# Kernel optimization log

Hardware: AMD Instinct MI355X
Metric: run time of the kernel (lower is better)

Reference implementation:

```python
import jax, jax.numpy as jnp
import numpy as np

D_MODEL = 64
HEADS = 8
LEVELS = 5
POINTS = 4
DH = D_MODEL // HEADS
EPS = 1e-5


def _layernorm(x, g, b):
    m = x.mean(-1, keepdims=True)
    v = ((x - m) ** 2).mean(-1, keepdims=True)
    return (x - m) / jnp.sqrt(v + EPS) * g + b


def _bilinear_sample(v, lx, ly, Hl, Wl):
    # v: (B, heads, Hl, Wl, dh); lx, ly: (B, Nq, heads, P) normalized in ~[0,1]
    # matches F.grid_sample(align_corners=False, padding_mode='zeros')
    x = lx * Wl - 0.5
    y = ly * Hl - 0.5
    x0 = jnp.floor(x)
    y0 = jnp.floor(y)
    wx = x - x0
    wy = y - y0
    x0i = x0.astype(jnp.int32)
    y0i = y0.astype(jnp.int32)
    B, heads = v.shape[0], v.shape[1]
    bidx = jnp.arange(B)[:, None, None, None]
    hidx = jnp.arange(heads)[None, None, :, None]

    def gather(yi, xi):
        valid = (xi >= 0) & (xi < Wl) & (yi >= 0) & (yi < Hl)
        xc = jnp.clip(xi, 0, Wl - 1)
        yc = jnp.clip(yi, 0, Hl - 1)
        g = v[bidx, hidx, yc, xc]  # (B, Nq, heads, P, dh)
        return g * valid[..., None].astype(v.dtype)

    return (gather(y0i, x0i) * ((1 - wx) * (1 - wy))[..., None]
            + gather(y0i, x0i + 1) * (wx * (1 - wy))[..., None]
            + gather(y0i + 1, x0i) * ((1 - wx) * wy)[..., None]
            + gather(y0i + 1, x0i + 1) * (wx * wy)[..., None])


def setup_inputs() -> dict:
    key = jax.random.key(0)
    ks = jax.random.split(key, 24)
    B, NQ = 2, 20000
    ss = np.array([[184, 184], [92, 92], [46, 46], [23, 23], [12, 12]], dtype=np.int64)
    areas = ss[:, 0] * ss[:, 1]
    lsi = np.concatenate([[0], np.cumsum(areas)[:-1]]).astype(np.int64)
    LIN = int(areas.sum())  # 45109
    s = 0.02
    inp = {
        'q_feat': jax.random.normal(ks[0], (B, NQ, D_MODEL), jnp.float32),
        'dense_voxel_flatten': jax.random.normal(ks[1], (B, LIN, D_MODEL), jnp.float32),
        'reference_points': jax.random.uniform(ks[2], (B, NQ, 2), jnp.float32),
        'q_pos': jax.random.normal(ks[3], (B, NQ, D_MODEL), jnp.float32),
        'spatial_shapes': ss,
        'level_start_index': lsi,
        'Wv': jax.random.normal(ks[4], (D_MODEL, D_MODEL), jnp.float32) * s,
        'bv': jnp.zeros((D_MODEL,), jnp.float32),
        'Wo': jax.random.normal(ks[5], (D_MODEL, HEADS * LEVELS * POINTS * 2), jnp.float32) * s,
        'bo': jax.random.normal(ks[6], (HEADS * LEVELS * POINTS * 2,), jnp.float32),
        'Wa': jax.random.normal(ks[7], (D_MODEL, HEADS * LEVELS * POINTS), jnp.float32) * s,
        'ba': jnp.zeros((HEADS * LEVELS * POINTS,), jnp.float32),
        'Wout': jax.random.normal(ks[8], (D_MODEL, D_MODEL), jnp.float32) * s,
        'bout': jnp.zeros((D_MODEL,), jnp.float32),
        'g1': jnp.ones((D_MODEL,), jnp.float32),
        'b1': jnp.zeros((D_MODEL,), jnp.float32),
        'W1': jax.random.normal(ks[9], (D_MODEL, 1024), jnp.float32) * s,
        'bff1': jnp.zeros((1024,), jnp.float32),
        'W2': jax.random.normal(ks[10], (1024, D_MODEL), jnp.float32) * s,
        'bff2': jnp.zeros((D_MODEL,), jnp.float32),
        'g2': jnp.ones((D_MODEL,), jnp.float32),
        'b2': jnp.zeros((D_MODEL,), jnp.float32),
    }
    return inp


def reference(q_feat, dense_voxel_flatten, reference_points, q_pos,
              spatial_shapes, level_start_index,
              Wv, bv, Wo, bo, Wa, ba, Wout, bout,
              g1, b1, W1, bff1, W2, bff2, g2, b2):
    B, NQ, _ = q_feat.shape
    q = q_feat + q_pos  # with_pos_embed
    value = (dense_voxel_flatten @ Wv + bv).reshape(B, -1, HEADS, DH)
    off = (q @ Wo + bo).reshape(B, NQ, HEADS, LEVELS, POINTS, 2)
    aw = jax.nn.softmax((q @ Wa + ba).reshape(B, NQ, HEADS, LEVELS * POINTS), axis=-1)
    aw = aw.reshape(B, NQ, HEADS, LEVELS, POINTS)
    # offset normalizer is (W, H) per level
    ssn = np.asarray(spatial_shapes)
    normalizer = jnp.asarray(ssn[:, ::-1].copy(), q.dtype)  # (L, 2)
    loc = reference_points[:, :, None, None, None, :] + off / normalizer[None, None, None, :, None, :]
    out = jnp.zeros((B, NQ, HEADS, DH), q.dtype)
    for l in range(LEVELS):
        Hl, Wl = int(ssn[l, 0]), int(ssn[l, 1])
        st = int(np.asarray(level_start_index)[l])
        vl = value[:, st:st + Hl * Wl].reshape(B, Hl, Wl, HEADS, DH).transpose(0, 3, 1, 2, 4)
        sampled = _bilinear_sample(vl, loc[:, :, :, l, :, 0], loc[:, :, :, l, :, 1], Hl, Wl)
        out = out + jnp.einsum('bnhpd,bnhp->bnhd', sampled, aw[:, :, :, l])
    attn_out = out.reshape(B, NQ, D_MODEL) @ Wout + bout
    x = _layernorm(q_feat + attn_out, g1, b1)  # residual + norm1 (dropout=0)
    ffn = jax.nn.relu(x @ W1 + bff1) @ W2 + bff2
    return _layernorm(x + ffn, g2, b2)
```

## Files before the change

kernel.cpp:

```cpp
#include <hip/hip_runtime.h>
#include <hip/hip_bf16.h>

#define NB 2
#define NQ 20000
#define DM 64
#define NH 8
#define NL 5
#define NP 4
#define LIN 45109
#define FFN 1024

typedef __attribute__((ext_vector_type(8))) short short8;
typedef __attribute__((ext_vector_type(4))) float f32x4;

__device__ __forceinline__ float b2f(const __hip_bfloat16 h) { return __bfloat162float(h); }
__device__ __forceinline__ float lo16f(unsigned u) { return __uint_as_float(u << 16); }
__device__ __forceinline__ float hi16f(unsigned u) { return __uint_as_float(u & 0xffff0000u); }
__device__ __forceinline__ unsigned f2bf_bits(float x) {
    unsigned u = __float_as_uint(x);
    return (u + 0x7FFFu + ((u >> 16) & 1u)) >> 16;
}

__global__ void __launch_bounds__(256)
val_proj_kernel(const float* __restrict__ dvf,
                const float* __restrict__ Wv,
                const float* __restrict__ bv,
                __hip_bfloat16* __restrict__ valA,
                __hip_bfloat16* __restrict__ valB,
                int rows) {
    __shared__ __align__(16) __hip_bfloat16 wvp[8][64][8];
    __shared__ __align__(16) __hip_bfloat16 ar[64][72];
    __shared__ __align__(16) float bvs[64];

    const int tid = threadIdx.x;
    const int lane = tid & 63;
    const int w = tid >> 6;
    const int m16 = lane & 15, qd = lane >> 4;
    const int row0 = blockIdx.x * 64;

    for (int idx = tid; idx < 4096; idx += 256) {
        const int j = idx & 7;
        const int l = (idx >> 3) & 63;
        const int seg = idx >> 9;
        const int nt = seg >> 1, kc = seg & 1;
        const int n = nt * 16 + (l & 15);
        const int k = kc * 32 + (l >> 4) * 8 + j;
        wvp[seg][l][j] = __float2bfloat16(Wv[k * 64 + n]);
    }
    if (tid < 64) bvs[tid] = bv[tid];

    {
        const int r = w * 16 + m16;
        const int grow = row0 + r;
        const int c0 = qd * 16;
        __hip_bfloat16* dst = &ar[r][c0];
        if (grow < rows) {
            const float4* src = (const float4*)&dvf[(size_t)grow * DM + c0];
#pragma unroll
            for (int t = 0; t < 4; t++) {
                const float4 v = src[t];
                dst[t * 4 + 0] = __float2bfloat16(v.x);
                dst[t * 4 + 1] = __float2bfloat16(v.y);
                dst[t * 4 + 2] = __float2bfloat16(v.z);
                dst[t * 4 + 3] = __float2bfloat16(v.w);
            }
        } else {
#pragma unroll
            for (int t = 0; t < 16; t++) dst[t] = __float2bfloat16(0.f);
        }
    }
    __syncthreads();

    f32x4 acc[4];
#pragma unroll
    for (int nt = 0; nt < 4; nt++) acc[nt] = (f32x4){0.f, 0.f, 0.f, 0.f};
#pragma unroll
    for (int kc = 0; kc < 2; kc++) {
        const short8 a = *(const short8*)&ar[w * 16 + m16][kc * 32 + qd * 8];
#pragma unroll
        for (int nt = 0; nt < 4; nt++) {
            const short8 b = *(const short8*)&wvp[nt * 2 + kc][lane][0];
            acc[nt] = __builtin_amdgcn_mfma_f32_16x16x32_bf16(a, b, acc[nt], 0, 0, 0);
        }
    }

#pragma unroll
    for (int r = 0; r < 4; r++) {
        const int gr = row0 + w * 16 + qd * 4 + r;
        if (gr < rows) {
            const int vr = (gr < LIN) ? gr : gr - LIN;
            __hip_bfloat16* dst = (gr < LIN) ? valA : valB;
#pragma unroll
            for (int nt = 0; nt < 4; nt++) {
                const int c = nt * 16 + m16;
                dst[((size_t)(c >> 3) * LIN + vr) * 8 + (c & 7)] =
                    __float2bfloat16(acc[nt][r] + bvs[c]);
            }
        }
    }
}

__global__ void pack_kernel(const float* __restrict__ W1, const float* __restrict__ W2,
                            const float* __restrict__ Wo, const float* __restrict__ Wa,
                            const float* __restrict__ Wout,
                            __hip_bfloat16* __restrict__ W1p, __hip_bfloat16* __restrict__ W2p,
                            __hip_bfloat16* __restrict__ Woap, __hip_bfloat16* __restrict__ Woutp) {
    const int t = blockIdx.x * 256 + threadIdx.x;
    const int lane = t & 63;
    const int m = lane & 15, qd = lane >> 4;
    const int seg = t >> 6;
    if (seg < 128) {
        const int nt = seg >> 1, kc = seg & 1;
        const int n = nt * 16 + m, kb = kc * 32 + qd * 8;
        __hip_bfloat16* dst = W1p + ((size_t)seg * 64 + lane) * 8;
#pragma unroll
        for (int j = 0; j < 8; j++) dst[j] = __float2bfloat16(W1[(size_t)(kb + j) * FFN + n]);
    } else if (seg < 256) {
        const int sl = seg - 128;
        const int nt = sl >> 5, kc = sl & 31;
        const int n = nt * 16 + m, kb = kc * 32 + qd * 8;
        __hip_bfloat16* dst = W2p + ((size_t)sl * 64 + lane) * 8;
#pragma unroll
        for (int j = 0; j < 8; j++) dst[j] = __float2bfloat16(W2[(size_t)(kb + j) * DM + n]);
    } else if (seg < 316) {
        const int sl = seg - 256;
        const int nt = sl >> 1, kc = sl & 1;
        const int n = nt * 16 + m, kb = kc * 32 + qd * 8;
        __hip_bfloat16* dst = Woap + ((size_t)sl * 64 + lane) * 8;
#pragma unroll
        for (int j = 0; j < 8; j++) {
            const int k = kb + j;
            const float v = (n < 320) ? Wo[(size_t)k * 320 + n] : Wa[(size_t)k * 160 + (n - 320)];
            dst[j] = __float2bfloat16(v);
        }
    } else if (seg < 324) {
        const int sl = seg - 316;
        const int nt = sl >> 1, kc = sl & 1;
        const int n = nt * 16 + m, kb = kc * 32 + qd * 8;
        __hip_bfloat16* dst = Woutp + ((size_t)sl * 64 + lane) * 8;
#pragma unroll
        for (int j = 0; j < 8; j++) dst[j] = __float2bfloat16(Wout[(size_t)(kb + j) * DM + n]);
    }
}

__global__ void __launch_bounds__(256, 8)
attn4_kernel(const float* __restrict__ q_feat,
             const float* __restrict__ ref_pts,
             const float* __restrict__ q_pos,
             const __hip_bfloat16* __restrict__ Woap,
             const float* __restrict__ bo, const float* __restrict__ ba,
             const __hip_bfloat16* __restrict__ Woutp, const float* __restrict__ bout,
             const float* __restrict__ g1, const float* __restrict__ b1,
             const __hip_bfloat16* __restrict__ valA,
             const __hip_bfloat16* __restrict__ valB,
             int qoff,
             float* __restrict__ xout) {
    __shared__ __align__(16) __hip_bfloat16 qb[16][72];
    __shared__ __align__(16) float offs[4][321];
    __shared__ __align__(16) float aws[4][161];
    __shared__ __align__(16) float refs[4][2];
    __shared__ __align__(16) int   dbase[640];
    __shared__ __align__(16) uint2 dwp[640];
    __shared__ __align__(16) float xs4[4][64];

    const int tid = threadIdx.x;
    const int lane = tid & 63;
    const int w = tid >> 6;
    const int m16 = lane & 15, qd = lane >> 4;
    const int q0 = qoff + blockIdx.x * 4;
    const int qi = q0 + w;

    const int sz[NL]  = {184, 92, 46, 23, 12};
    const int lsi[NL] = {0, 33856, 42320, 44436, 44965};

    const __hip_bfloat16* valp = (q0 >= NQ) ? valB : valA;

    const float qf = q_feat[(size_t)qi * DM + lane];
    const float qp = q_pos[(size_t)qi * DM + lane];
    qb[w][lane] = __float2bfloat16(qf + qp);
    for (int idx = tid; idx < 12 * 64; idx += 256)
        qb[4 + (idx >> 6)][idx & 63] = __float2bfloat16(0.f);
    if (tid < 8) refs[tid >> 1][tid & 1] = ref_pts[(size_t)(q0 + (tid >> 1)) * 2 + (tid & 1)];
    __syncthreads();

    for (int nt = w; nt < 30; nt += 4) {
        f32x4 acc = {0.f, 0.f, 0.f, 0.f};
#pragma unroll
        for (int kc = 0; kc < 2; kc++) {
            const short8 a = *(const short8*)&qb[m16][kc * 32 + qd * 8];
            const short8 b = *(const short8*)(Woap + ((size_t)(nt * 2 + kc) * 64 + lane) * 8);
            acc = __builtin_amdgcn_mfma_f32_16x16x32_bf16(a, b, acc, 0, 0, 0);
        }
        if (qd == 0) {
            const int n = nt * 16 + m16;
            if (n < 320) {
                const float bn = bo[n];
#pragma unroll
                for (int r = 0; r < 4; r++) offs[r][n] = acc[r] + bn;
            } else {
                const float bn = ba[n - 320];
#pragma unroll
                for (int r = 0; r < 4; r++) aws[r][n - 320] = acc[r] + bn;
            }
        }
    }
    __syncthreads();

    {
        const int g = tid >> 3;
        const int q = g >> 3, h = g & 7;
        const int j = tid & 7;
        float* p = &aws[q][h * 20];
        const float v0 = p[j], v1 = p[j + 8];
        const float v2 = (j < 4) ? p[j + 16] : -1e30f;
        float mx = fmaxf(fmaxf(v0, v1), v2);
        mx = fmaxf(mx, __shfl_xor(mx, 1, 8));
        mx = fmaxf(mx, __shfl_xor(mx, 2, 8));
        mx = fmaxf(mx, __shfl_xor(mx, 4, 8));
        const float e0 = __expf(v0 - mx), e1 = __expf(v1 - mx);
        const float e2 = (j < 4) ? __expf(v2 - mx) : 0.f;
        float s = e0 + e1 + e2;
        s += __shfl_xor(s, 1, 8);
        s += __shfl_xor(s, 2, 8);
        s += __shfl_xor(s, 4, 8);
        const float inv = 1.f / s;
        p[j] = e0 * inv;
        p[j + 8] = e1 * inv;
        if (j < 4) p[j + 16] = e2 * inv;
    }
    __syncthreads();

    for (int s = tid; s < 640; s += 256) {
        const int h = s & 7;
        const int t2 = s >> 3;
        const int p = t2 & 3;
        const int t3 = t2 >> 2;
        const int l = t3 % 5;
        const int q = t3 / 5;
        const int Wl = sz[l];
        const float Wf = (float)Wl;
        const int st = lsi[l];
        const int c = ((h * 5 + l) * 4 + p) * 2;
        const float fx = fmaf(refs[q][0], Wf, offs[q][c]) - 0.5f;
        const float fy = fmaf(refs[q][1], Wf, offs[q][c + 1]) - 0.5f;
        const float x0f = floorf(fx), y0f = floorf(fy);
        const float wx = fx - x0f, wy = fy - y0f;
        const int x0 = (int)x0f, y0 = (int)y0f;
        const float aV = aws[q][h * 20 + l * 4 + p];
        const bool xin0 = (x0 >= 0) & (x0 < Wl);
        const bool xin1 = (x0 >= -1) & (x0 < Wl - 1);
        const bool yin0 = (y0 >= 0) & (y0 < Wl);
        const bool yin1 = (y0 >= -1) & (y0 < Wl - 1);
        const float w00 = (xin0 & yin0) ? (1.f - wx) * (1.f - wy) * aV : 0.f;
        const float w10 = (xin1 & yin0) ? wx * (1.f - wy) * aV : 0.f;
        const float w01 = (xin0 & yin1) ? (1.f - wx) * wy * aV : 0.f;
        const float w11 = (xin1 & yin1) ? wx * wy * aV : 0.f;
        int base = (st + y0 * Wl + x0) * 8;
        base = base < -1520 ? -1520 : base;
        base = base > LIN * 8 ? LIN * 8 : base;
        dbase[s] = base;
        uint2 dw;
        dw.x = f2bf_bits(w00) | (f2bf_bits(w10) << 16);
        dw.y = f2bf_bits(w01) | (f2bf_bits(w11) << 16);
        dwp[s] = dw;
    }
    __syncthreads();

    {
        const int h = lane >> 3, d = lane & 7;
        const __hip_bfloat16* vbase = valp + (size_t)h * (LIN * 8) + d;
        float a0 = 0.f, a1 = 0.f, a2 = 0.f, a3 = 0.f;
        const int wl8[NL] = {184 * 8, 92 * 8, 46 * 8, 23 * 8, 12 * 8};
#pragma unroll
        for (int l = 0; l < NL; l++) {
#pragma unroll
            for (int p = 0; p < NP; p++) {
                const int idx = ((w * 5 + l) * 4 + p) * 8 + h;
                const int base = dbase[idx];
                const uint2 dw = dwp[idx];
                const __hip_bfloat16* r0 = vbase + base;
                const __hip_bfloat16* r1 = r0 + wl8[l];
                a0 = fmaf(lo16f(dw.x), b2f(r0[0]), a0);
                a1 = fmaf(hi16f(dw.x), b2f(r0[8]), a1);
                a2 = fmaf(lo16f(dw.y), b2f(r1[0]), a2);
                a3 = fmaf(hi16f(dw.y), b2f(r1[8]), a3);
            }
        }
        qb[w][lane] = __float2bfloat16((a0 + a1) + (a2 + a3));
    }
    __syncthreads();

    {
        f32x4 acc = {0.f, 0.f, 0.f, 0.f};
#pragma unroll
        for (int kc = 0; kc < 2; kc++) {
            const short8 a = *(const short8*)&qb[m16][kc * 32 + qd * 8];
            const short8 b = *(const short8*)(Woutp + ((size_t)(w * 2 + kc) * 64 + lane) * 8);
            acc = __builtin_amdgcn_mfma_f32_16x16x32_bf16(a, b, acc, 0, 0, 0);
        }
        if (qd == 0) {
            const int n = w * 16 + m16;
            const float bn = bout[n];
#pragma unroll
            for (int r = 0; r < 4; r++) xs4[r][n] = acc[r] + bn;
        }
    }
    __syncthreads();

    {
        const float xpre = qf + xs4[w][lane];
        float s = xpre, s2 = xpre * xpre;
#pragma unroll
        for (int o = 32; o >= 1; o >>= 1) {
            s += __shfl_xor(s, o, 64);
            s2 += __shfl_xor(s2, o, 64);
        }
        const float mean = s * (1.f / 64.f);
        const float var = s2 * (1.f / 64.f) - mean * mean;
        const float xn = (xpre - mean) * rsqrtf(var + 1e-5f);
        xout[(size_t)qi * DM + lane] = xn * g1[lane] + b1[lane];
    }
}

__global__ void __launch_bounds__(256)
ffn_kernel(const __hip_bfloat16* __restrict__ W1p, const float* __restrict__ bff1,
           const __hip_bfloat16* __restrict__ W2p, const float* __restrict__ bff2,
           const float* __restrict__ g2, const float* __restrict__ b2,
           float* __restrict__ io) {
    __shared__ __align__(16) __hip_bfloat16 xb[32][72];
    __shared__ __align__(16) __hip_bfloat16 hb[32][264];
    __shared__ __align__(16) float yr[32][64];

    const int tid = threadIdx.x;
    const int lane = tid & 63;
    const int w = tid >> 6;
    const int m16 = lane & 15, qd = lane >> 4;
    const int q0 = blockIdx.x * 32;

    {
        const int q = tid >> 3, i = tid & 7;
        const float4 v0 = *(const float4*)&io[(size_t)(q0 + q) * DM + i * 8];
        const float4 v1 = *(const float4*)&io[(size_t)(q0 + q) * DM + i * 8 + 4];
        __hip_bfloat16* xp = &xb[q][i * 8];
        xp[0] = __float2bfloat16(v0.x); xp[1] = __float2bfloat16(v0.y);
        xp[2] = __float2bfloat16(v0.z); xp[3] = __float2bfloat16(v0.w);
        xp[4] = __float2bfloat16(v1.x); xp[5] = __float2bfloat16(v1.y);
        xp[6] = __float2bfloat16(v1.z); xp[7] = __float2bfloat16(v1.w);
    }
    __syncthreads();

    f32x4 yacc[2];
    yacc[0] = (f32x4){0.f, 0.f, 0.f, 0.f};
    yacc[1] = (f32x4){0.f, 0.f, 0.f, 0.f};

#pragma unroll
    for (int qtr = 0; qtr < 4; qtr++) {
#pragma unroll
        for (int ti = 0; ti < 4; ti++) {
            const int nt = qtr * 16 + w + ti * 4;
            f32x4 acc[2];
            acc[0] = (f32x4){0.f, 0.f, 0.f, 0.f};
            acc[1] = (f32x4){0.f, 0.f, 0.f, 0.f};
#pragma unroll
            for (int kc = 0; kc < 2; kc++) {
                const short8 b = *(const short8*)(W1p + ((size_t)(nt * 2 + kc) * 64 + lane) * 8);
#pragma unroll
                for (int mt = 0; mt < 2; mt++) {
                    const short8 a = *(const short8*)&xb[mt * 16 + m16][kc * 32 + qd * 8];
                    acc[mt] = __builtin_amdgcn_mfma_f32_16x16x32_bf16(a, b, acc[mt], 0, 0, 0);
                }
            }
            const int ncol = (nt - qtr * 16) * 16 + m16;
            const float bn = bff1[nt * 16 + m16];
#pragma unroll
            for (int mt = 0; mt < 2; mt++)
#pragma unroll
                for (int r = 0; r < 4; r++)
                    hb[mt * 16 + qd * 4 + r][ncol] = __float2bfloat16(fmaxf(acc[mt][r] + bn, 0.f));
        }
        __syncthreads();
#pragma unroll
        for (int kc2 = 0; kc2 < 8; kc2++) {
            const short8 b = *(const short8*)(W2p + ((size_t)(w * 32 + qtr * 8 + kc2) * 64 + lane) * 8);
#pragma unroll
            for (int mt = 0; mt < 2; mt++) {
                const short8 a = *(const short8*)&hb[mt * 16 + m16][kc2 * 32 + qd * 8];
                yacc[mt] = __builtin_amdgcn_mfma_f32_16x16x32_bf16(a, b, yacc[mt], 0, 0, 0);
            }
        }
        __syncthreads();
    }

    {
        const int n = w * 16 + m16;
        const float bn = bff2[n];
#pragma unroll
        for (int mt = 0; mt < 2; mt++)
#pragma unroll
            for (int r = 0; r < 4; r++) {
                const int mm = mt * 16 + qd * 4 + r;
                yr[mm][n] = yacc[mt][r] + bn;
            }
    }
    __syncthreads();

    {
        const int q = tid >> 3, i = tid & 7;
        const float4 x0 = *(const float4*)&io[(size_t)(q0 + q) * DM + i * 8];
        const float4 x1 = *(const float4*)&io[(size_t)(q0 + q) * DM + i * 8 + 4];
        float4 v0 = *(const float4*)&yr[q][i * 8];
        float4 v1 = *(const float4*)&yr[q][i * 8 + 4];
        v0.x += x0.x; v0.y += x0.y; v0.z += x0.z; v0.w += x0.w;
        v1.x += x1.x; v1.y += x1.y; v1.z += x1.z; v1.w += x1.w;
        float s = v0.x + v0.y + v0.z + v0.w + v1.x + v1.y + v1.z + v1.w;
        float s2 = v0.x * v0.x + v0.y * v0.y + v0.z * v0.z + v0.w * v0.w
                 + v1.x * v1.x + v1.y * v1.y + v1.z * v1.z + v1.w * v1.w;
#pragma unroll
        for (int o = 4; o >= 1; o >>= 1) { s += __shfl_xor(s, o, 64); s2 += __shfl_xor(s2, o, 64); }
        const float mean = s * (1.f / 64.f);
        const float var = s2 * (1.f / 64.f) - mean * mean;
        const float rstd = rsqrtf(var + 1e-5f);
        const float4 ga = *(const float4*)&g2[i * 8];
        const float4 gb = *(const float4*)&g2[i * 8 + 4];
        const float4 ba4 = *(const float4*)&b2[i * 8];
        const float4 bb4 = *(const float4*)&b2[i * 8 + 4];
        float4 o0, o1;
        o0.x = (v0.x - mean) * rstd * ga.x + ba4.x;
        o0.y = (v0.y - mean) * rstd * ga.y + ba4.y;
        o0.z = (v0.z - mean) * rstd * ga.z + ba4.z;
        o0.w = (v0.w - mean) * rstd * ga.w + ba4.w;
        o1.x = (v1.x - mean) * rstd * gb.x + bb4.x;
        o1.y = (v1.y - mean) * rstd * gb.y + bb4.y;
        o1.z = (v1.z - mean) * rstd * gb.z + bb4.z;
        o1.w = (v1.w - mean) * rstd * gb.w + bb4.w;
        *(float4*)&io[(size_t)(q0 + q) * DM + i * 8] = o0;
        *(float4*)&io[(size_t)(q0 + q) * DM + i * 8 + 4] = o1;
    }
}

extern "C" void kernel_launch(void* const* d_in, const int* in_sizes, int n_in,
                              void* d_out, int out_size, void* d_ws, size_t ws_size,
                              hipStream_t stream) {
    const int B0 = (in_sizes[4] >= 4096) ? 4 : 6;
    const float* q_feat = (const float*)d_in[0];
    const float* dvf    = (const float*)d_in[1];
    const float* refp   = (const float*)d_in[2];
    const float* q_pos  = (const float*)d_in[3];
    const float* Wv   = (const float*)d_in[B0 + 0];
    const float* bv   = (const float*)d_in[B0 + 1];
    const float* Wo   = (const float*)d_in[B0 + 2];
    const float* bo   = (const float*)d_in[B0 + 3];
    const float* Wa   = (const float*)d_in[B0 + 4];
    const float* ba   = (const float*)d_in[B0 + 5];
    const float* Wout = (const float*)d_in[B0 + 6];
    const float* bout = (const float*)d_in[B0 + 7];
    const float* g1   = (const float*)d_in[B0 + 8];
    const float* b1   = (const float*)d_in[B0 + 9];
    const float* W1   = (const float*)d_in[B0 + 10];
    const float* bff1 = (const float*)d_in[B0 + 11];
    const float* W2   = (const float*)d_in[B0 + 12];
    const float* bff2 = (const float*)d_in[B0 + 13];
    const float* g2   = (const float*)d_in[B0 + 14];
    const float* b2   = (const float*)d_in[B0 + 15];
    float* out = (float*)d_out;

    const size_t val_elems = (size_t)LIN * DM;
    const size_t pack_elems = (size_t)(128 + 128 + 60 + 8) * 64 * 8;
    const size_t PAD_ELEMS = 12288;
    const bool dbuf = ws_size >= (pack_elems + 2 * val_elems + PAD_ELEMS) * sizeof(__hip_bfloat16);

    __hip_bfloat16* W1p = (__hip_bfloat16*)d_ws;
    __hip_bfloat16* W2p = W1p + (size_t)128 * 64 * 8;
    __hip_bfloat16* Woap = W2p + (size_t)128 * 64 * 8;
    __hip_bfloat16* Woutp = Woap + (size_t)60 * 64 * 8;
    __hip_bfloat16* val0 = W1p + pack_elems;
    __hip_bfloat16* val1 = dbuf ? val0 + val_elems : val0;

    __hip_bfloat16* pad_ptr = val1 + val_elems;
    hipMemsetAsync(pad_ptr, 0, PAD_ELEMS * sizeof(__hip_bfloat16), stream);

    pack_kernel<<<81, 256, 0, stream>>>(W1, W2, Wo, Wa, Wout, W1p, W2p, Woap, Woutp);

    if (dbuf) {
        val_proj_kernel<<<(2 * LIN + 63) / 64, 256, 0, stream>>>(
            dvf, Wv, bv, val0, val1, 2 * LIN);
        attn4_kernel<<<(NB * NQ) / 4, 256, 0, stream>>>(
            q_feat, refp, q_pos, Woap, bo, ba, Woutp, bout, g1, b1,
            val0, val1, 0, out);
    } else {
        for (int b = 0; b < NB; b++) {
            val_proj_kernel<<<(LIN + 63) / 64, 256, 0, stream>>>(
                dvf + (size_t)b * val_elems, Wv, bv, val0, val0, LIN);
            attn4_kernel<<<NQ / 4, 256, 0, stream>>>(
                q_feat, refp, q_pos, Woap, bo, ba, Woutp, bout, g1, b1,
                val0, val0, b * NQ, out);
        }
    }
    ffn_kernel<<<(NB * NQ) / 32, 256, 0, stream>>>(W1p, bff1, W2p, bff2, g2, b2, out);
}
```

Baseline: 251.3 us.

## Vectorize bilinear corner gathers to 16-byte loads with shuffle reduction

Before, each lane loaded one bf16 per corner, 80 scalar gathers in total. Now each lane loads a full 8-channel bf16 vector for one corner of one sample point, so each query-head needs 10 wide loads. Partial sums are combined with xor shuffles across 8 lanes and a select. The per-sample descriptor is packed into a single int4 and xs4 is aliased onto offs to cut LDS use. In exchange, 8-wide accumulators add register pressure and 24 shuffles per lane are added.

```diff
diff --git a/kernel.cpp b/kernel.cpp
--- a/kernel.cpp
+++ b/kernel.cpp
@@ -159,9 +159,9 @@
     __shared__ __align__(16) float offs[4][321];
     __shared__ __align__(16) float aws[4][161];
     __shared__ __align__(16) float refs[4][2];
-    __shared__ __align__(16) int   dbase[640];
-    __shared__ __align__(16) uint2 dwp[640];
-    __shared__ __align__(16) float xs4[4][64];
+    __shared__ __align__(16) int4  dsc[640];
+
+    float (*xs4)[64] = (float(*)[64])offs;
 
     const int tid = threadIdx.x;
     const int lane = tid & 63;
@@ -255,38 +255,46 @@
         const float w10 = (xin1 & yin0) ? wx * (1.f - wy) * aV : 0.f;
         const float w01 = (xin0 & yin1) ? (1.f - wx) * wy * aV : 0.f;
         const float w11 = (xin1 & yin1) ? wx * wy * aV : 0.f;
-        int base = (st + y0 * Wl + x0) * 8;
-        base = base < -1520 ? -1520 : base;
-        base = base > LIN * 8 ? LIN * 8 : base;
-        dbase[s] = base;
-        uint2 dw;
-        dw.x = f2bf_bits(w00) | (f2bf_bits(w10) << 16);
-        dw.y = f2bf_bits(w01) | (f2bf_bits(w11) << 16);
-        dwp[s] = dw;
-    }
-    __syncthreads();
-
-    {
-        const int h = lane >> 3, d = lane & 7;
-        const __hip_bfloat16* vbase = valp + (size_t)h * (LIN * 8) + d;
-        float a0 = 0.f, a1 = 0.f, a2 = 0.f, a3 = 0.f;
-        const int wl8[NL] = {184 * 8, 92 * 8, 46 * 8, 23 * 8, 12 * 8};
-#pragma unroll
-        for (int l = 0; l < NL; l++) {
-#pragma unroll
-            for (int p = 0; p < NP; p++) {
-                const int idx = ((w * 5 + l) * 4 + p) * 8 + h;
-                const int base = dbase[idx];
-                const uint2 dw = dwp[idx];
-                const __hip_bfloat16* r0 = vbase + base;
-                const __hip_bfloat16* r1 = r0 + wl8[l];
-                a0 = fmaf(lo16f(dw.x), b2f(r0[0]), a0);
-                a1 = fmaf(hi16f(dw.x), b2f(r0[8]), a1);
-                a2 = fmaf(lo16f(dw.y), b2f(r1[0]), a2);
-                a3 = fmaf(hi16f(dw.y), b2f(r1[8]), a3);
-            }
-        }
-        qb[w][lane] = __float2bfloat16((a0 + a1) + (a2 + a3));
+        int b0 = (st + y0 * Wl + x0) * 8;
+        b0 = b0 < -1520 ? -1520 : b0;
+        b0 = b0 > LIN * 8 ? LIN * 8 : b0;
+        const int b1 = b0 + Wl * 8;
+        int4 d4;
+        d4.x = b0;
+        d4.y = b1;
+        d4.z = (int)(f2bf_bits(w00) | (f2bf_bits(w10) << 16));
+        d4.w = (int)(f2bf_bits(w01) | (f2bf_bits(w11) << 16));
+        dsc[s] = d4;
+    }
+    __syncthreads();
+
+    {
+        const int h = lane >> 3, j = lane & 7;
+        const int c = j & 3;
+        const int sp = j >> 2;
+        const __hip_bfloat16* vbase = valp + (size_t)h * (LIN * 8);
+        float acc[8] = {0.f, 0.f, 0.f, 0.f, 0.f, 0.f, 0.f, 0.f};
+#pragma unroll
+        for (int k = 0; k < 10; k++) {
+            const int s = 2 * k + sp;
+            const int4 d4 = dsc[(w * 20 + s) * 8 + h];
+            const int base = (c >= 2) ? d4.y : d4.x;
+            const unsigned wb = (unsigned)((c >= 2) ? d4.w : d4.z);
+            const float wt = (c & 1) ? hi16f(wb) : lo16f(wb);
+            const short8 v = *(const short8*)(vbase + base + (c & 1) * 8);
+#pragma unroll
+            for (int d = 0; d < 8; d++)
+                acc[d] = fmaf(wt, __uint_as_float(((unsigned)(unsigned short)v[d]) << 16), acc[d]);
+        }
+#pragma unroll
+        for (int o = 1; o <= 4; o <<= 1)
+#pragma unroll
+            for (int d = 0; d < 8; d++)
+                acc[d] += __shfl_xor(acc[d], o, 64);
+        float r = acc[0];
+#pragma unroll
+        for (int d = 1; d < 8; d++) r = (j == d) ? acc[d] : r;
+        qb[w][lane] = __float2bfloat16(r);
     }
     __syncthreads();
 
```

Result: faster. 236.4 us (-5.9%).
